# Kernel tuning notes

Hardware: AMD Instinct MI355X
Metric: run time of the kernel (lower is better)

Reference implementation:

```python
import jax, jax.numpy as jnp
import numpy as np

SHORT_LEN = 10
NEG_INF = -1.0e9


def _attn_pool(values, user, w, w_bias, extra_b, mask, softmax_axis):
    # values: [B,L,D], user: [B,D]; linear+bias+relu, dot with user, masked softmax, weighted sum
    h = jax.nn.relu(jnp.einsum('bld,ed->ble', values, w) + w_bias + extra_b)
    s = jnp.einsum('bld,bd->bl', h, user)
    s = jnp.where(mask, NEG_INF, s)
    a = jax.nn.softmax(s, axis=softmax_axis)
    return jnp.einsum('bld,bl->bd', values, a)


def setup_inputs() -> dict:
    key = jax.random.key(0)
    ks = jax.random.split(key, 10)
    B, L, D, NI, NU = 2048, 50, 64, 100000, 100000
    return {
        'seq': jax.random.randint(ks[0], (B, L), 0, NI),
        'user_id': jax.random.randint(ks[1], (B,), 0, NU),
        'item_emb': jax.random.normal(ks[2], (NI, D), jnp.float32) * 0.01,
        'user_emb': jax.random.normal(ks[3], (NU, D), jnp.float32) * 0.01,
        'long_w': jax.random.normal(ks[4], (D, D), jnp.float32) * 0.1,
        'long_w_bias': jax.random.normal(ks[5], (D,), jnp.float32) * 0.1,
        'long_b': jax.random.normal(ks[6], (D,), jnp.float32) * 0.1,
        'long_short_w': jax.random.normal(ks[7], (D, D), jnp.float32) * 0.1,
        'long_short_w_bias': jax.random.normal(ks[8], (D,), jnp.float32) * 0.1,
        'long_short_b': jax.random.normal(ks[9], (D,), jnp.float32) * 0.1,
    }


def reference(seq, user_id, item_emb, user_emb, long_w, long_w_bias, long_b,
              long_short_w, long_short_w_bias, long_short_b):
    e = item_emb[seq]                     # [B,L,D]
    u = user_emb[user_id]                 # [B,D]
    mask = seq == 0                       # padding mask
    # long-term attention pooling (softmax over dim=1)
    long_term = _attn_pool(e, u, long_w, long_w_bias, long_b, mask, 1)[:, None, :]  # [B,1,D]
    # concat long-term summary with last SHORT_LEN items
    short = e[:, -SHORT_LEN:, :]
    mask_ls = jnp.concatenate([jnp.zeros((seq.shape[0], 1), bool), mask[:, -SHORT_LEN:]], axis=1)
    ls = jnp.concatenate([long_term, short], axis=1)  # [B,1+K,D]
    pooled = _attn_pool(ls, u, long_short_w, long_short_w_bias, long_short_b, mask_ls, -1)  # [B,D]
    scores = pooled @ item_emb.T          # [B, n_items]
    return scores
```

## Files before the change

kernel.cpp:

```cpp
#include <hip/hip_runtime.h>
#include <hip/hip_bf16.h>


#define L_SEQ 50
#define D_EMB 64
#define SHORT_LEN 10
#define LS_LEN 11
#define NEG_INF_F (-1000000000.0f)
#define TILE_STRIP 16

typedef __bf16 bf16x8 __attribute__((ext_vector_type(8)));
typedef float f32x4 __attribute__((ext_vector_type(4)));

__device__ __forceinline__ float wave_sum(float v) {
#pragma unroll
  for (int off = 32; off > 0; off >>= 1) v += __shfl_xor(v, off, 64);
  return v;
}
__device__ __forceinline__ float wave_max(float v) {
#pragma unroll
  for (int off = 32; off > 0; off >>= 1) v = fmaxf(v, __shfl_xor(v, off, 64));
  return v;
}

__global__ __launch_bounds__(64) void pool_kernel(
    const int* __restrict__ seq, const int* __restrict__ user_id,
    const float* __restrict__ item_emb, const float* __restrict__ user_emb,
    const float* __restrict__ w1, const float* __restrict__ w1b, const float* __restrict__ b1,
    const float* __restrict__ w2, const float* __restrict__ w2b, const float* __restrict__ b2,
    float* __restrict__ pooled_f32, __bf16* __restrict__ pooled_bf) {
  const int b = blockIdx.x;
  const int lane = threadIdx.x;

  __shared__ float e_lds[L_SEQ][D_EMB];
  __shared__ float ls_lds[LS_LEN][D_EMB];
  __shared__ float a_lds[D_EMB];
  __shared__ int seq_lds[L_SEQ];

  if (lane < L_SEQ) seq_lds[lane] = seq[b * L_SEQ + lane];
  const float u = user_emb[(long)user_id[b] * D_EMB + lane];
  __syncthreads();

  for (int l = 0; l < L_SEQ; ++l) {
    e_lds[l][lane] = item_emb[(long)seq_lds[l] * D_EMB + lane];
  }

  float4 w1r[16];
#pragma unroll
  for (int k = 0; k < 16; ++k) w1r[k] = *(const float4*)&w1[lane * D_EMB + 4 * k];
  const float bias1 = w1b[lane] + b1[lane];
  __syncthreads();

  float s_val = 0.0f;
  for (int l = 0; l < L_SEQ; ++l) {
    float acc = bias1;
#pragma unroll
    for (int k = 0; k < 16; ++k) {
      float4 ev = *(const float4*)&e_lds[l][4 * k];
      acc = fmaf(ev.x, w1r[k].x, acc);
      acc = fmaf(ev.y, w1r[k].y, acc);
      acc = fmaf(ev.z, w1r[k].z, acc);
      acc = fmaf(ev.w, w1r[k].w, acc);
    }
    acc = fmaxf(acc, 0.0f);
    float t = wave_sum(acc * u);
    if (lane == l) s_val = (seq_lds[l] == 0) ? NEG_INF_F : t;
  }
  {
    float x = (lane < L_SEQ) ? s_val : -INFINITY;
    float m = wave_max(x);
    float p = (lane < L_SEQ) ? __expf(x - m) : 0.0f;
    float ps = wave_sum(p);
    a_lds[lane] = p / ps;
  }
  __syncthreads();

  float lt = 0.0f;
  for (int l = 0; l < L_SEQ; ++l) lt = fmaf(a_lds[l], e_lds[l][lane], lt);
  __syncthreads();

  ls_lds[0][lane] = lt;
#pragma unroll
  for (int j = 1; j < LS_LEN; ++j)
    ls_lds[j][lane] = e_lds[L_SEQ - SHORT_LEN + (j - 1)][lane];

  float4 w2r[16];
#pragma unroll
  for (int k = 0; k < 16; ++k) w2r[k] = *(const float4*)&w2[lane * D_EMB + 4 * k];
  const float bias2 = w2b[lane] + b2[lane];
  __syncthreads();

  float s2_val = 0.0f;
  for (int j = 0; j < LS_LEN; ++j) {
    float acc = bias2;
#pragma unroll
    for (int k = 0; k < 16; ++k) {
      float4 lv = *(const float4*)&ls_lds[j][4 * k];
      acc = fmaf(lv.x, w2r[k].x, acc);
      acc = fmaf(lv.y, w2r[k].y, acc);
      acc = fmaf(lv.z, w2r[k].z, acc);
      acc = fmaf(lv.w, w2r[k].w, acc);
    }
    acc = fmaxf(acc, 0.0f);
    float t = wave_sum(acc * u);
    bool msk = (j == 0) ? false : (seq_lds[L_SEQ - SHORT_LEN + (j - 1)] == 0);
    if (lane == j) s2_val = msk ? NEG_INF_F : t;
  }
  {
    float x = (lane < LS_LEN) ? s2_val : -INFINITY;
    float m = wave_max(x);
    float p = (lane < LS_LEN) ? __expf(x - m) : 0.0f;
    float ps = wave_sum(p);
    __syncthreads();
    a_lds[lane] = p / ps;
  }
  __syncthreads();

  float po = 0.0f;
#pragma unroll
  for (int j = 0; j < LS_LEN; ++j) po = fmaf(a_lds[j], ls_lds[j][lane], po);
  if (pooled_f32) pooled_f32[(long)b * D_EMB + lane] = po;
  if (pooled_bf) pooled_bf[(long)b * D_EMB + lane] = (__bf16)po;
}

__global__ __launch_bounds__(256) void cvt_bf16_kernel(
    const float* __restrict__ in, __bf16* __restrict__ out, int n8) {
  int i = blockIdx.x * blockDim.x + threadIdx.x;
  if (i >= n8) return;
  float4 a = ((const float4*)in)[2 * i];
  float4 b = ((const float4*)in)[2 * i + 1];
  bf16x8 v;
  v[0] = (__bf16)a.x; v[1] = (__bf16)a.y; v[2] = (__bf16)a.z; v[3] = (__bf16)a.w;
  v[4] = (__bf16)b.x; v[5] = (__bf16)b.y; v[6] = (__bf16)b.z; v[7] = (__bf16)b.w;
  ((bf16x8*)out)[i] = v;
}

__global__ __launch_bounds__(256) void scores_mfma_kernel(
    const __bf16* __restrict__ pooled_bf,
    const __bf16* __restrict__ item_bf,
    float* __restrict__ out, int NI, int n_tiles) {
  const int tid = threadIdx.x;
  const int w = tid >> 6;
  const int l = tid & 63;
  const int lr = l & 15;
  const int lg = l >> 4;
  const int b0 = blockIdx.y * 256 + w * 64;

  bf16x8 pfrag[4][2];
#pragma unroll
  for (int g = 0; g < 4; ++g) {
    const __bf16* prow = pooled_bf + (size_t)(b0 + 16 * g + lr) * D_EMB + 8 * lg;
    pfrag[g][0] = *(const bf16x8*)(prow);
    pfrag[g][1] = *(const bf16x8*)(prow + 32);
  }

  const int t_begin = blockIdx.x * TILE_STRIP;
  const int t_end = min(t_begin + TILE_STRIP, n_tiles);

#pragma unroll 2
  for (int t = t_begin; t < t_end; ++t) {
    const __bf16* brow = item_bf + (size_t)(t * 16 + lr) * D_EMB + 8 * lg;
    bf16x8 a0 = *(const bf16x8*)(brow);
    bf16x8 a1 = *(const bf16x8*)(brow + 32);

#pragma unroll
    for (int g = 0; g < 4; ++g) {
      f32x4 acc = {0.f, 0.f, 0.f, 0.f};
      acc = __builtin_amdgcn_mfma_f32_16x16x32_bf16(a0, pfrag[g][0], acc, 0, 0, 0);
      acc = __builtin_amdgcn_mfma_f32_16x16x32_bf16(a1, pfrag[g][1], acc, 0, 0, 0);
      float* op = out + (size_t)(b0 + 16 * g + lr) * NI + t * 16 + 4 * lg;
      __builtin_nontemporal_store(acc, (f32x4*)op);
    }
  }
}

__global__ __launch_bounds__(256) void scores_kernel(
    const float* __restrict__ pooled, const float* __restrict__ item_emb,
    float* __restrict__ out, int NI) {
  constexpr int STR = 68;
  __shared__ __align__(16) float poolT[64 * STR];
  __shared__ __align__(16) float itemT[64 * STR];

  const int tid = threadIdx.x;
  const int lane = tid & 63;
  const int b0 = blockIdx.x * 64;
  const int i0 = blockIdx.y * 64;

  for (int r = tid >> 6; r < 64; r += 4) {
    poolT[lane * STR + r] = pooled[(long)(b0 + r) * D_EMB + lane];
    int i = i0 + r;
    itemT[lane * STR + r] = (i < NI) ? item_emb[(long)i * D_EMB + lane] : 0.0f;
  }
  __syncthreads();

  const int tx = tid & 15;
  const int ty = tid >> 4;
  float acc[4][4] = {};

#pragma unroll 8
  for (int d = 0; d < 64; ++d) {
    float4 pv = *(const float4*)&poolT[d * STR + ty * 4];
    float4 iv = *(const float4*)&itemT[d * STR + tx * 4];
    float pva[4] = {pv.x, pv.y, pv.z, pv.w};
    float iva[4] = {iv.x, iv.y, iv.z, iv.w};
#pragma unroll
    for (int m = 0; m < 4; ++m)
#pragma unroll
      for (int n = 0; n < 4; ++n) acc[m][n] = fmaf(pva[m], iva[n], acc[m][n]);
  }

  const int ibase = i0 + tx * 4;
  const long orow = (long)(b0 + ty * 4);
  if (i0 + 63 < NI) {
#pragma unroll
    for (int m = 0; m < 4; ++m) {
      float4 v = make_float4(acc[m][0], acc[m][1], acc[m][2], acc[m][3]);
      *(float4*)&out[(orow + m) * (long)NI + ibase] = v;
    }
  } else {
#pragma unroll
    for (int m = 0; m < 4; ++m)
#pragma unroll
      for (int n = 0; n < 4; ++n)
        if (ibase + n < NI) out[(orow + m) * (long)NI + ibase + n] = acc[m][n];
  }
}

extern "C" void kernel_launch(void* const* d_in, const int* in_sizes, int n_in,
                              void* d_out, int out_size, void* d_ws, size_t ws_size,
                              hipStream_t stream) {
  const int* seq = (const int*)d_in[0];
  const int* user_id = (const int*)d_in[1];
  const float* item_emb = (const float*)d_in[2];
  const float* user_emb = (const float*)d_in[3];
  const float* w1 = (const float*)d_in[4];
  const float* w1b = (const float*)d_in[5];
  const float* b1 = (const float*)d_in[6];
  const float* w2 = (const float*)d_in[7];
  const float* w2b = (const float*)d_in[8];
  const float* b2 = (const float*)d_in[9];
  float* out = (float*)d_out;

  const int B = in_sizes[1];
  const int NI = in_sizes[2] / D_EMB;

  const size_t item_bf_bytes = (size_t)NI * D_EMB * 2;
  const size_t pooled_bf_bytes = (size_t)B * D_EMB * 2;
  const bool mfma_ok = (ws_size >= item_bf_bytes + pooled_bf_bytes) &&
                       (NI % 16 == 0) && (B % 256 == 0) && (D_EMB == 64);

  if (mfma_ok) {
    __bf16* item_bf = (__bf16*)d_ws;
    __bf16* pooled_bf = (__bf16*)((char*)d_ws + item_bf_bytes);

    const int n8 = NI * D_EMB / 8;
    cvt_bf16_kernel<<<(n8 + 255) / 256, 256, 0, stream>>>(item_emb, item_bf, n8);

    pool_kernel<<<B, 64, 0, stream>>>(seq, user_id, item_emb, user_emb,
                                      w1, w1b, b1, w2, w2b, b2,
                                      (float*)nullptr, pooled_bf);

    const int n_tiles = NI / 16;
    dim3 grid((n_tiles + TILE_STRIP - 1) / TILE_STRIP, B / 256);
    scores_mfma_kernel<<<grid, 256, 0, stream>>>(pooled_bf, item_bf, out, NI, n_tiles);
  } else {
    float* pooled = (float*)d_ws;
    pool_kernel<<<B, 64, 0, stream>>>(seq, user_id, item_emb, user_emb,
                                      w1, w1b, b1, w2, w2b, b2,
                                      pooled, (__bf16*)nullptr);
    dim3 grid(B / 64, (NI + 63) / 64);
    scores_kernel<<<grid, 256, 0, stream>>>(pooled, item_emb, out, NI);
  }
}
```

Baseline: 310.6 us.

## Remap score-GEMM blocks across XCDs and batch eight tile loads per block

The scores kernel now runs on a 1D grid whose block index is remapped so the 8 batch-row groups for one item strip land on the same XCD, which lets them share the item tiles in that XCD's L2. Each block handles a strip of 8 item tiles. It loads all 8 tiles up front, then issues the MFMAs and stores, giving more memory-level parallelism per block. A tail path covers partial strips, and the fast path is gated to B/256 == 8. The costs are higher register use and less generality for other batch sizes.

```diff
diff --git a/kernel.cpp b/kernel.cpp
--- a/kernel.cpp
+++ b/kernel.cpp
@@ -7,7 +7,7 @@
 #define SHORT_LEN 10
 #define LS_LEN 11
 #define NEG_INF_F (-1000000000.0f)
-#define TILE_STRIP 16
+#define TC 8
 
 typedef __bf16 bf16x8 __attribute__((ext_vector_type(8)));
 typedef float f32x4 __attribute__((ext_vector_type(4)));
@@ -138,13 +138,19 @@
 __global__ __launch_bounds__(256) void scores_mfma_kernel(
     const __bf16* __restrict__ pooled_bf,
     const __bf16* __restrict__ item_bf,
-    float* __restrict__ out, int NI, int n_tiles) {
+    float* __restrict__ out, int NI, int n_tiles, int n_strips) {
+  const int n = blockIdx.x;
+  const int xcd = n & 7;
+  const int y = (n >> 3) & 7;
+  const int s = (n >> 6) * 8 + xcd;
+  if (s >= n_strips) return;
+
   const int tid = threadIdx.x;
   const int w = tid >> 6;
   const int l = tid & 63;
   const int lr = l & 15;
   const int lg = l >> 4;
-  const int b0 = blockIdx.y * 256 + w * 64;
+  const int b0 = y * 256 + w * 64;
 
   bf16x8 pfrag[4][2];
 #pragma unroll
@@ -154,22 +160,45 @@
     pfrag[g][1] = *(const bf16x8*)(prow + 32);
   }
 
-  const int t_begin = blockIdx.x * TILE_STRIP;
-  const int t_end = min(t_begin + TILE_STRIP, n_tiles);
-
-#pragma unroll 2
-  for (int t = t_begin; t < t_end; ++t) {
-    const __bf16* brow = item_bf + (size_t)(t * 16 + lr) * D_EMB + 8 * lg;
-    bf16x8 a0 = *(const bf16x8*)(brow);
-    bf16x8 a1 = *(const bf16x8*)(brow + 32);
-
+  const int t0 = s * TC;
+  const int tcnt = min(TC, n_tiles - t0);
+
+  if (tcnt == TC) {
+    bf16x8 af0[TC], af1[TC];
+#pragma unroll
+    for (int tt = 0; tt < TC; ++tt) {
+      const __bf16* brow = item_bf + (size_t)((t0 + tt) * 16 + lr) * D_EMB + 8 * lg;
+      af0[tt] = *(const bf16x8*)(brow);
+      af1[tt] = *(const bf16x8*)(brow + 32);
+    }
 #pragma unroll
     for (int g = 0; g < 4; ++g) {
-      f32x4 acc = {0.f, 0.f, 0.f, 0.f};
-      acc = __builtin_amdgcn_mfma_f32_16x16x32_bf16(a0, pfrag[g][0], acc, 0, 0, 0);
-      acc = __builtin_amdgcn_mfma_f32_16x16x32_bf16(a1, pfrag[g][1], acc, 0, 0, 0);
-      float* op = out + (size_t)(b0 + 16 * g + lr) * NI + t * 16 + 4 * lg;
-      __builtin_nontemporal_store(acc, (f32x4*)op);
+      f32x4 acc[TC];
+#pragma unroll
+      for (int tt = 0; tt < TC; ++tt) {
+        f32x4 a = {0.f, 0.f, 0.f, 0.f};
+        a = __builtin_amdgcn_mfma_f32_16x16x32_bf16(af0[tt], pfrag[g][0], a, 0, 0, 0);
+        a = __builtin_amdgcn_mfma_f32_16x16x32_bf16(af1[tt], pfrag[g][1], a, 0, 0, 0);
+        acc[tt] = a;
+      }
+      float* op = out + (size_t)(b0 + 16 * g + lr) * NI + t0 * 16 + 4 * lg;
+#pragma unroll
+      for (int tt = 0; tt < TC; ++tt)
+        __builtin_nontemporal_store(acc[tt], (f32x4*)(op + tt * 16));
+    }
+  } else {
+    for (int t = t0; t < t0 + tcnt; ++t) {
+      const __bf16* brow = item_bf + (size_t)(t * 16 + lr) * D_EMB + 8 * lg;
+      bf16x8 a0 = *(const bf16x8*)(brow);
+      bf16x8 a1 = *(const bf16x8*)(brow + 32);
+#pragma unroll
+      for (int g = 0; g < 4; ++g) {
+        f32x4 acc = {0.f, 0.f, 0.f, 0.f};
+        acc = __builtin_amdgcn_mfma_f32_16x16x32_bf16(a0, pfrag[g][0], acc, 0, 0, 0);
+        acc = __builtin_amdgcn_mfma_f32_16x16x32_bf16(a1, pfrag[g][1], acc, 0, 0, 0);
+        float* op = out + (size_t)(b0 + 16 * g + lr) * NI + t * 16 + 4 * lg;
+        __builtin_nontemporal_store(acc, (f32x4*)op);
+      }
     }
   }
 }
@@ -247,7 +276,8 @@
   const size_t item_bf_bytes = (size_t)NI * D_EMB * 2;
   const size_t pooled_bf_bytes = (size_t)B * D_EMB * 2;
   const bool mfma_ok = (ws_size >= item_bf_bytes + pooled_bf_bytes) &&
-                       (NI % 16 == 0) && (B % 256 == 0) && (D_EMB == 64);
+                       (NI % 16 == 0) && (B % 256 == 0) && (D_EMB == 64) &&
+                       (B / 256 == 8);
 
   if (mfma_ok) {
     __bf16* item_bf = (__bf16*)d_ws;
@@ -261,8 +291,10 @@
                                       (float*)nullptr, pooled_bf);
 
     const int n_tiles = NI / 16;
-    dim3 grid((n_tiles + TILE_STRIP - 1) / TILE_STRIP, B / 256);
-    scores_mfma_kernel<<<grid, 256, 0, stream>>>(pooled_bf, item_bf, out, NI, n_tiles);
+    const int n_strips = (n_tiles + TC - 1) / TC;
+    const int nblocks = ((n_strips + 7) / 8) * 64;
+    scores_mfma_kernel<<<nblocks, 256, 0, stream>>>(pooled_bf, item_bf, out,
+                                                    NI, n_tiles, n_strips);
   } else {
     float* pooled = (float*)d_ws;
     pool_kernel<<<B, 64, 0, stream>>>(seq, user_id, item_emb, user_emb,
```

Result: slower. 323.5 us (+4.2%).

## Stage MFMA score tiles in LDS for fully coalesced row-contiguous output stores

Applied to the files above, without the earlier changes.

Rewrites the scores kernel so each block computes a 16-user by 1024-item chunk. Each wave writes its MFMA accumulators into a swizzled shared-memory stage, then after a barrier the block writes whole contiguous row segments of the output. Before, each lane wrote scattered 16-byte pieces across 16 rows. The goal is better write coalescing for the 800 MB output, which dominates runtime. In exchange, each block now reuses the pooled fragments across far fewer items, so the item table is read many more times (once per 16-user group rather than once per 256-user group). It also adds a 64 KB shared-memory buffer that limits occupancy and drops the nontemporal store hint.

```diff
diff --git a/kernel.cpp b/kernel.cpp
--- a/kernel.cpp
+++ b/kernel.cpp
@@ -7,7 +7,8 @@
 #define SHORT_LEN 10
 #define LS_LEN 11
 #define NEG_INF_F (-1000000000.0f)
-#define TILE_STRIP 16
+#define CHUNK_TILES 64
+#define CHUNK_I (CHUNK_TILES * 16)
 
 typedef __bf16 bf16x8 __attribute__((ext_vector_type(8)));
 typedef float f32x4 __attribute__((ext_vector_type(4)));
@@ -138,38 +139,53 @@
 __global__ __launch_bounds__(256) void scores_mfma_kernel(
     const __bf16* __restrict__ pooled_bf,
     const __bf16* __restrict__ item_bf,
-    float* __restrict__ out, int NI, int n_tiles) {
+    float* __restrict__ out, int NI, int n_tiles, int n_groups) {
+  __shared__ float stage[16][CHUNK_I];
+
+  const int chunk = blockIdx.x / n_groups;
+  const int bg = blockIdx.x % n_groups;
   const int tid = threadIdx.x;
   const int w = tid >> 6;
   const int l = tid & 63;
   const int lr = l & 15;
   const int lg = l >> 4;
-  const int b0 = blockIdx.y * 256 + w * 64;
-
-  bf16x8 pfrag[4][2];
-#pragma unroll
-  for (int g = 0; g < 4; ++g) {
-    const __bf16* prow = pooled_bf + (size_t)(b0 + 16 * g + lr) * D_EMB + 8 * lg;
-    pfrag[g][0] = *(const bf16x8*)(prow);
-    pfrag[g][1] = *(const bf16x8*)(prow + 32);
-  }
-
-  const int t_begin = blockIdx.x * TILE_STRIP;
-  const int t_end = min(t_begin + TILE_STRIP, n_tiles);
-
-#pragma unroll 2
-  for (int t = t_begin; t < t_end; ++t) {
+  const int b0 = bg * 16;
+
+  const int i0 = chunk * CHUNK_I;
+  const int ilen = min(CHUNK_I, NI - i0);
+
+  const __bf16* prow = pooled_bf + (size_t)(b0 + lr) * D_EMB + 8 * lg;
+  bf16x8 pf0 = *(const bf16x8*)(prow);
+  bf16x8 pf1 = *(const bf16x8*)(prow + 32);
+
+  const int tl_cnt = min(16, ilen / 16 - w * 16);
+#pragma unroll 4
+  for (int tt = 0; tt < tl_cnt; ++tt) {
+    const int t = chunk * CHUNK_TILES + w * 16 + tt;
     const __bf16* brow = item_bf + (size_t)(t * 16 + lr) * D_EMB + 8 * lg;
     bf16x8 a0 = *(const bf16x8*)(brow);
     bf16x8 a1 = *(const bf16x8*)(brow + 32);
-
-#pragma unroll
-    for (int g = 0; g < 4; ++g) {
-      f32x4 acc = {0.f, 0.f, 0.f, 0.f};
-      acc = __builtin_amdgcn_mfma_f32_16x16x32_bf16(a0, pfrag[g][0], acc, 0, 0, 0);
-      acc = __builtin_amdgcn_mfma_f32_16x16x32_bf16(a1, pfrag[g][1], acc, 0, 0, 0);
-      float* op = out + (size_t)(b0 + 16 * g + lr) * NI + t * 16 + 4 * lg;
-      __builtin_nontemporal_store(acc, (f32x4*)op);
+    f32x4 acc = {0.f, 0.f, 0.f, 0.f};
+    acc = __builtin_amdgcn_mfma_f32_16x16x32_bf16(a0, pf0, acc, 0, 0, 0);
+    acc = __builtin_amdgcn_mfma_f32_16x16x32_bf16(a1, pf1, acc, 0, 0, 0);
+    const int G = (w * 16 + tt) * 4 + lg;
+    const int Gp = G ^ (lr & 7);
+    *(f32x4*)&stage[lr][Gp * 4] = acc;
+  }
+  __syncthreads();
+
+#pragma unroll
+  for (int q = 0; q < 4; ++q) {
+    const int row = w * 4 + q;
+    float* orow = out + (size_t)(b0 + row) * NI + i0;
+#pragma unroll
+    for (int c = 0; c < CHUNK_I / 256; ++c) {
+      const int G = c * 64 + l;
+      if (G * 4 < ilen) {
+        const int Gp = G ^ (row & 7);
+        f32x4 v = *(const f32x4*)&stage[row][Gp * 4];
+        *(f32x4*)&orow[G * 4] = v;
+      }
     }
   }
 }
@@ -247,7 +263,7 @@
   const size_t item_bf_bytes = (size_t)NI * D_EMB * 2;
   const size_t pooled_bf_bytes = (size_t)B * D_EMB * 2;
   const bool mfma_ok = (ws_size >= item_bf_bytes + pooled_bf_bytes) &&
-                       (NI % 16 == 0) && (B % 256 == 0) && (D_EMB == 64);
+                       (NI % 32 == 0) && (B % 16 == 0) && (D_EMB == 64);
 
   if (mfma_ok) {
     __bf16* item_bf = (__bf16*)d_ws;
@@ -261,8 +277,10 @@
                                       (float*)nullptr, pooled_bf);
 
     const int n_tiles = NI / 16;
-    dim3 grid((n_tiles + TILE_STRIP - 1) / TILE_STRIP, B / 256);
-    scores_mfma_kernel<<<grid, 256, 0, stream>>>(pooled_bf, item_bf, out, NI, n_tiles);
+    const int n_chunks = (n_tiles + CHUNK_TILES - 1) / CHUNK_TILES;
+    const int n_groups = B / 16;
+    scores_mfma_kernel<<<n_chunks * n_groups, 256, 0, stream>>>(
+        pooled_bf, item_bf, out, NI, n_tiles, n_groups);
   } else {
     float* pooled = (float*)d_ws;
     pool_kernel<<<B, 64, 0, stream>>>(seq, user_id, item_emb, user_emb,
```

Result: slower. 464.3 us (+49.5%).

## Stage MFMA score tiles in LDS for coalesced row-contiguous output stores

Applied to the files above, without the earlier changes.

Each wave now computes one 16-row batch group across a 256-item strip, writing MFMA results into a swizzled LDS buffer. The buffer is then written out as full contiguous 1 KB row segments per wave. This targets the scattered 64-byte row-strided stores of the huge score matrix. In exchange, item tiles are reloaded once per 64 batch rows instead of per 256, a block barrier is added, and nontemporal stores are dropped.

```diff
diff --git a/kernel.cpp b/kernel.cpp
--- a/kernel.cpp
+++ b/kernel.cpp
@@ -7,7 +7,8 @@
 #define SHORT_LEN 10
 #define LS_LEN 11
 #define NEG_INF_F (-1000000000.0f)
-#define TILE_STRIP 16
+#define STRIP_TILES 16
+#define STRIP_I 256
 
 typedef __bf16 bf16x8 __attribute__((ext_vector_type(8)));
 typedef float f32x4 __attribute__((ext_vector_type(4)));
@@ -138,38 +139,50 @@
 __global__ __launch_bounds__(256) void scores_mfma_kernel(
     const __bf16* __restrict__ pooled_bf,
     const __bf16* __restrict__ item_bf,
-    float* __restrict__ out, int NI, int n_tiles) {
+    float* __restrict__ out, int NI, int n_tiles, int n_bgrp) {
+  __shared__ __align__(16) float stage[4][16][STRIP_I];
+
+  const int bid = blockIdx.x;
+  const int strip = bid / n_bgrp;
+  const int bq = bid % n_bgrp;
   const int tid = threadIdx.x;
   const int w = tid >> 6;
   const int l = tid & 63;
   const int lr = l & 15;
   const int lg = l >> 4;
-  const int b0 = blockIdx.y * 256 + w * 64;
-
-  bf16x8 pfrag[4][2];
-#pragma unroll
-  for (int g = 0; g < 4; ++g) {
-    const __bf16* prow = pooled_bf + (size_t)(b0 + 16 * g + lr) * D_EMB + 8 * lg;
-    pfrag[g][0] = *(const bf16x8*)(prow);
-    pfrag[g][1] = *(const bf16x8*)(prow + 32);
-  }
-
-  const int t_begin = blockIdx.x * TILE_STRIP;
-  const int t_end = min(t_begin + TILE_STRIP, n_tiles);
-
-#pragma unroll 2
-  for (int t = t_begin; t < t_end; ++t) {
-    const __bf16* brow = item_bf + (size_t)(t * 16 + lr) * D_EMB + 8 * lg;
+  const int b0 = (bq * 4 + w) * 16;
+
+  const int t0 = strip * STRIP_TILES;
+  const int tl_cnt = min(STRIP_TILES, n_tiles - t0);
+  const int i0 = t0 * 16;
+  const int ilen = min(STRIP_I, NI - i0);
+
+  const __bf16* prow = pooled_bf + (size_t)(b0 + lr) * D_EMB + 8 * lg;
+  bf16x8 pf0 = *(const bf16x8*)(prow);
+  bf16x8 pf1 = *(const bf16x8*)(prow + 32);
+
+  float(*st)[STRIP_I] = stage[w];
+
+#pragma unroll 4
+  for (int tt = 0; tt < tl_cnt; ++tt) {
+    const __bf16* brow = item_bf + (size_t)((t0 + tt) * 16 + lr) * D_EMB + 8 * lg;
     bf16x8 a0 = *(const bf16x8*)(brow);
     bf16x8 a1 = *(const bf16x8*)(brow + 32);
-
-#pragma unroll
-    for (int g = 0; g < 4; ++g) {
-      f32x4 acc = {0.f, 0.f, 0.f, 0.f};
-      acc = __builtin_amdgcn_mfma_f32_16x16x32_bf16(a0, pfrag[g][0], acc, 0, 0, 0);
-      acc = __builtin_amdgcn_mfma_f32_16x16x32_bf16(a1, pfrag[g][1], acc, 0, 0, 0);
-      float* op = out + (size_t)(b0 + 16 * g + lr) * NI + t * 16 + 4 * lg;
-      __builtin_nontemporal_store(acc, (f32x4*)op);
+    f32x4 acc = {0.f, 0.f, 0.f, 0.f};
+    acc = __builtin_amdgcn_mfma_f32_16x16x32_bf16(a0, pf0, acc, 0, 0, 0);
+    acc = __builtin_amdgcn_mfma_f32_16x16x32_bf16(a1, pf1, acc, 0, 0, 0);
+    const int gp = (tt * 4 + lg) ^ (lr & 7);
+    *(f32x4*)&st[lr][gp * 4] = acc;
+  }
+  __syncthreads();
+
+  const bool full = (4 * l < ilen);
+#pragma unroll 4
+  for (int r = 0; r < 16; ++r) {
+    if (full) {
+      const int gp = l ^ (r & 7);
+      f32x4 v = *(const f32x4*)&st[r][gp * 4];
+      *(f32x4*)&out[(size_t)(b0 + r) * NI + i0 + 4 * l] = v;
     }
   }
 }
@@ -247,7 +260,7 @@
   const size_t item_bf_bytes = (size_t)NI * D_EMB * 2;
   const size_t pooled_bf_bytes = (size_t)B * D_EMB * 2;
   const bool mfma_ok = (ws_size >= item_bf_bytes + pooled_bf_bytes) &&
-                       (NI % 16 == 0) && (B % 256 == 0) && (D_EMB == 64);
+                       (NI % 16 == 0) && (B % 64 == 0) && (D_EMB == 64);
 
   if (mfma_ok) {
     __bf16* item_bf = (__bf16*)d_ws;
@@ -261,8 +274,10 @@
                                       (float*)nullptr, pooled_bf);
 
     const int n_tiles = NI / 16;
-    dim3 grid((n_tiles + TILE_STRIP - 1) / TILE_STRIP, B / 256);
-    scores_mfma_kernel<<<grid, 256, 0, stream>>>(pooled_bf, item_bf, out, NI, n_tiles);
+    const int n_strips = (n_tiles + STRIP_TILES - 1) / STRIP_TILES;
+    const int n_bgrp = B / 64;
+    scores_mfma_kernel<<<n_strips * n_bgrp, 256, 0, stream>>>(
+        pooled_bf, item_bf, out, NI, n_tiles, n_bgrp);
   } else {
     float* pooled = (float*)d_ws;
     pool_kernel<<<B, 64, 0, stream>>>(seq, user_id, item_emb, user_emb,
```

New measurement: 442.2 us. 42.4% more time.
